# Optimization experiments

Hardware: AMD Instinct MI355X
Metric: run time of the kernel (lower is better)

Reference implementation:

```python
import jax, jax.numpy as jnp
import numpy as np

C = 512
NUM_HEADS = 8
HEAD_DIM = C // NUM_HEADS
GROUPS = 32
EPS = 1e-5


def setup_inputs() -> dict:
    key = jax.random.key(0)
    ks = jax.random.split(key, 7)
    N, H, W = 16, 32, 32
    x = jax.random.normal(ks[0], (N, C, H, W), dtype=jnp.float32)
    norm_w = jax.random.normal(ks[1], (C,), dtype=jnp.float32) * 0.02 + 1.0
    norm_b = jax.random.normal(ks[2], (C,), dtype=jnp.float32) * 0.02
    qkv_w = jax.random.normal(ks[3], (3 * C, C), dtype=jnp.float32) * (1.0 / np.sqrt(C))
    qkv_b = jax.random.normal(ks[4], (3 * C,), dtype=jnp.float32) * 0.02
    proj_w = jax.random.normal(ks[5], (C, C), dtype=jnp.float32) * (1.0 / np.sqrt(C))
    proj_b = jax.random.normal(ks[6], (C,), dtype=jnp.float32) * 0.02
    return {"x": x, "norm_w": norm_w, "norm_b": norm_b, "qkv_w": qkv_w,
            "qkv_b": qkv_b, "proj_w": proj_w, "proj_b": proj_b}


def _group_norm(x, w, b):
    N, Cc, H, W = x.shape
    xg = x.reshape(N, GROUPS, Cc // GROUPS, H, W)
    mean = xg.mean(axis=(2, 3, 4), keepdims=True)
    var = xg.var(axis=(2, 3, 4), keepdims=True)
    xg = (xg - mean) * jax.lax.rsqrt(var + EPS)
    return xg.reshape(N, Cc, H, W) * w[None, :, None, None] + b[None, :, None, None]


def reference(x, norm_w, norm_b, qkv_w, qkv_b, proj_w, proj_b):
    N, Cc, H, W = x.shape
    S = H * W
    h = _group_norm(x, norm_w, norm_b)
    # 1x1 conv == per-pixel linear over channels
    qkv = jnp.einsum('nchw,oc->nohw', h, qkv_w) + qkv_b[None, :, None, None]
    q, k, v = jnp.split(qkv, 3, axis=1)  # each [N, C, H, W]
    # [N, heads, head_dim, S]
    q = q.reshape(N, NUM_HEADS, HEAD_DIM, S)
    k = k.reshape(N, NUM_HEADS, HEAD_DIM, S)
    v = v.reshape(N, NUM_HEADS, HEAD_DIM, S)
    scale = HEAD_DIM ** -0.5
    attn = jnp.einsum('nhds,nhdt->nhst', q, k) * scale  # [N,heads,S,S]
    attn = jax.nn.softmax(attn, axis=-1)
    out = jnp.einsum('nhst,nhdt->nhds', attn, v)  # [N,heads,head_dim,S]
    out = out.reshape(N, Cc, H, W)
    out = jnp.einsum('nchw,oc->nohw', out, proj_w) + proj_b[None, :, None, None]
    return out + x
```

## Files before the change

### kernel.cpp

```cpp
#include <hip/hip_runtime.h>
#include <cstdint>
#include <cstddef>

typedef unsigned short u16;
typedef __attribute__((ext_vector_type(8))) short bf16x8;
typedef __attribute__((ext_vector_type(4))) short bf16x4;
typedef __attribute__((ext_vector_type(4))) float f32x4;
typedef __attribute__((ext_vector_type(16))) float f32x16;
typedef __attribute__((ext_vector_type(4))) unsigned short u16x4;

#define NB 16
#define CD 512
#define SD 1024
#define NH 8
#define HD 64

__device__ __forceinline__ u16 f2bf(float f) {
    unsigned u = __float_as_uint(f);
    u += 0x7FFF + ((u >> 16) & 1);
    return (u16)(u >> 16);
}
__device__ __forceinline__ unsigned cvt_pk(float lo, float hi) {
    unsigned r;
    asm("v_cvt_pk_bf16_f32 %0, %1, %2" : "=v"(r) : "v"(lo), "v"(hi));
    return r;
}
__device__ __forceinline__ void gload16(const void* g, void* l) {
    __builtin_amdgcn_global_load_lds(
        (const __attribute__((address_space(1))) void*)g,
        (__attribute__((address_space(3))) void*)l, 16, 0, 0);
}

__global__ __launch_bounds__(256) void cvt_kernel(
    const float* __restrict__ s, u16* __restrict__ d, int n)
{
    int i = (blockIdx.x * 256 + threadIdx.x) * 4;
    if (i >= n) return;
    float4 v = *reinterpret_cast<const float4*>(s + i);
    u16x4 o = { f2bf(v.x), f2bf(v.y), f2bf(v.z), f2bf(v.w) };
    *reinterpret_cast<u16x4*>(d + i) = o;
}

__global__ __launch_bounds__(256) void gn_kernel(
    const float* __restrict__ x, const float* __restrict__ w,
    const float* __restrict__ b, u16* __restrict__ h)
{
    const int n = blockIdx.x >> 5, g = blockIdx.x & 31;
    const size_t base = ((size_t)n * CD + g * 16) * SD;
    const float4* xp = reinterpret_cast<const float4*>(x + base);

    float4 vals[16];
    float sum = 0.f, ss = 0.f;
#pragma unroll
    for (int i = 0; i < 16; ++i) {
        float4 v = xp[threadIdx.x + (i << 8)];
        vals[i] = v;
        sum += v.x + v.y + v.z + v.w;
        ss  += v.x*v.x + v.y*v.y + v.z*v.z + v.w*v.w;
    }
#pragma unroll
    for (int off = 32; off > 0; off >>= 1) {
        sum += __shfl_down(sum, off);
        ss  += __shfl_down(ss,  off);
    }
    __shared__ float rs[4], rq[4];
    const int wid = threadIdx.x >> 6, lane = threadIdx.x & 63;
    if (lane == 0) { rs[wid] = sum; rq[wid] = ss; }
    __syncthreads();
    const float tsum = rs[0] + rs[1] + rs[2] + rs[3];
    const float tss  = rq[0] + rq[1] + rq[2] + rq[3];
    const float mean = tsum * (1.0f / 16384.0f);
    const float var  = tss * (1.0f / 16384.0f) - mean * mean;
    const float inv  = rsqrtf(var + 1e-5f);

    u16* hp = h + ((size_t)n * SD + 4 * threadIdx.x) * CD + g * 16;
#pragma unroll
    for (int i = 0; i < 16; ++i) {
        const float A  = inv * w[g * 16 + i];
        const float Bc = b[g * 16 + i] - mean * A;
        float4 v = vals[i];
        hp[i]          = f2bf(v.x * A + Bc);
        hp[CD + i]     = f2bf(v.y * A + Bc);
        hp[2 * CD + i] = f2bf(v.z * A + Bc);
        hp[3 * CD + i] = f2bf(v.w * A + Bc);
    }
}

__global__ __launch_bounds__(256) void mfma_gemm(
    const u16* __restrict__ Wb, const u16* __restrict__ act,
    const float* __restrict__ bias, const float* __restrict__ resid,
    void* __restrict__ outp, u16* __restrict__ vtout, int M, int mode)
{
    const int nb = blockIdx.z, m0 = blockIdx.y * 128, s0 = blockIdx.x * 128;
    __shared__ u16 Al[128 * 64];
    __shared__ u16 Bl[128 * 64];
    const int tid = threadIdx.x, wv = tid >> 6, ln = tid & 63;
    const int wm = wv >> 1, wn = wv & 1, lr = ln & 15, lg = ln >> 4;

    const f32x4 zero = {0.f, 0.f, 0.f, 0.f};
    f32x4 acc[4][4];
#pragma unroll
    for (int i = 0; i < 4; ++i)
#pragma unroll
        for (int j = 0; j < 4; ++j) acc[i][j] = zero;

    const u16* Ab = Wb + (size_t)m0 * CD;
    const u16* Bb = act + ((size_t)nb * SD + s0) * CD;

    for (int k0 = 0; k0 < CD; k0 += 64) {
        __syncthreads();
#pragma unroll
        for (int r = 0; r < 4; ++r) {
            const int gi = (r * 4 + wv) * 64 + ln;
            const int row = gi >> 3, gc = gi & 7;
            const int sg = ((gc ^ (row & 7)) * 8);
            gload16(Ab + (size_t)row * CD + k0 + sg, Al + gi * 8);
            gload16(Bb + (size_t)row * CD + k0 + sg, Bl + gi * 8);
        }
        __syncthreads();

        bf16x8 af[4][2], bfr[4][2];
#pragma unroll
        for (int mi = 0; mi < 4; ++mi) {
            const int row = wm * 64 + mi * 16 + lr;
#pragma unroll
            for (int kc = 0; kc < 2; ++kc)
                af[mi][kc] = *reinterpret_cast<const bf16x8*>(
                    Al + row * 64 + (((kc * 4 + lg) ^ (row & 7)) * 8));
        }
#pragma unroll
        for (int nj = 0; nj < 4; ++nj) {
            const int row = wn * 64 + nj * 16 + lr;
#pragma unroll
            for (int kc = 0; kc < 2; ++kc)
                bfr[nj][kc] = *reinterpret_cast<const bf16x8*>(
                    Bl + row * 64 + (((kc * 4 + lg) ^ (row & 7)) * 8));
        }
#pragma unroll
        for (int kc = 0; kc < 2; ++kc)
#pragma unroll
            for (int mi = 0; mi < 4; ++mi)
#pragma unroll
                for (int nj = 0; nj < 4; ++nj)
                    acc[mi][nj] = __builtin_amdgcn_mfma_f32_16x16x32_bf16(
                        af[mi][kc], bfr[nj][kc], acc[mi][nj], 0, 0, 0);
    }

    if (mode == 0) {
        if (m0 < 1024) {
            u16* o = (u16*)outp;
#pragma unroll
            for (int mi = 0; mi < 4; ++mi)
#pragma unroll
                for (int r = 0; r < 4; ++r) {
                    const int m = m0 + wm * 64 + mi * 16 + lg * 4 + r;
                    const float bi = bias[m];
#pragma unroll
                    for (int nj = 0; nj < 4; ++nj) {
                        const int s = s0 + wn * 64 + nj * 16 + lr;
                        o[((size_t)nb * SD + s) * 1024 + m] = f2bf(acc[mi][nj][r] + bi);
                    }
                }
        } else {
#pragma unroll
            for (int mi = 0; mi < 4; ++mi)
#pragma unroll
                for (int r = 0; r < 4; ++r) {
                    const int m = m0 + wm * 64 + mi * 16 + lg * 4 + r;
                    const float bi = bias[m];
#pragma unroll
                    for (int nj = 0; nj < 4; ++nj) {
                        const int s = s0 + wn * 64 + nj * 16 + lr;
                        vtout[((size_t)nb * 512 + (m - 1024)) * SD + s] = f2bf(acc[mi][nj][r] + bi);
                    }
                }
        }
    } else {
        float* o = (float*)outp;
#pragma unroll
        for (int mi = 0; mi < 4; ++mi)
#pragma unroll
            for (int r = 0; r < 4; ++r) {
                const int m = m0 + wm * 64 + mi * 16 + lg * 4 + r;
                const float bi = bias[m];
#pragma unroll
                for (int nj = 0; nj < 4; ++nj) {
                    const int s = s0 + wn * 64 + nj * 16 + lr;
                    const size_t idx = ((size_t)nb * M + m) * SD + s;
                    o[idx] = acc[mi][nj][r] + bi + resid[idx];
                }
            }
    }
}

__global__ __launch_bounds__(512) void attn_mfma(
    const u16* __restrict__ qk, const u16* __restrict__ vt, u16* __restrict__ ao)
{
    const int nh = blockIdx.y, n = nh >> 3, hh = nh & 7;
    const int q0 = blockIdx.x << 8;
    const int tid = threadIdx.x, wv = tid >> 6, ln = tid & 63;
    const int lq = ln & 31, hi = ln >> 5;

    __shared__ u16 Kl[2][64 * 64];
    __shared__ u16 Vl[2][64 * 64];

    const u16* Qb = qk + (size_t)n * SD * 1024 + hh * HD;
    const u16* Kb = Qb + 512;
    const u16* Vb = vt + ((size_t)n * 512 + hh * HD) * SD;

    bf16x8 qf[4];
    {
        const u16* qp = Qb + (size_t)(q0 + wv * 32 + lq) * 1024 + hi * 8;
#pragma unroll
        for (int ks = 0; ks < 4; ++ks)
            qf[ks] = *reinterpret_cast<const bf16x8*>(qp + ks * 16);
    }

    f32x16 of0 = {}, of1 = {};
    float mrun = -INFINITY, lrun = 0.f;

    const int srow = tid >> 3, sgc = tid & 7;
    const int ssw = (sgc ^ (srow & 7)) * 8;
    const u16* Ksrc = Kb + (size_t)srow * 1024 + ssw;
    const u16* Vsrc = Vb + (size_t)srow * SD + ssw;

    gload16(Ksrc, &Kl[0][tid * 8]);
    gload16(Vsrc, &Vl[0][tid * 8]);
    __syncthreads();

    int cur = 0;
    for (int tt = 0; tt < 16; ++tt) {
        if (tt < 15) {
            const int t1 = (tt + 1) << 6;
            gload16(Ksrc + (size_t)t1 * 1024, &Kl[cur ^ 1][tid * 8]);
            gload16(Vsrc + t1, &Vl[cur ^ 1][tid * 8]);
        }
        f32x16 st0 = {}, st1 = {};
        const u16* Kc = &Kl[cur][0];
#pragma unroll
        for (int ks = 0; ks < 4; ++ks) {
            const int g = (((ks * 2 + hi) ^ (lq & 7)) * 8);
            bf16x8 k0 = *reinterpret_cast<const bf16x8*>(Kc + lq * 64 + g);
            bf16x8 k1 = *reinterpret_cast<const bf16x8*>(Kc + (32 + lq) * 64 + g);
            st0 = __builtin_amdgcn_mfma_f32_32x32x16_bf16(k0, qf[ks], st0, 0, 0, 0);
            st1 = __builtin_amdgcn_mfma_f32_32x32x16_bf16(k1, qf[ks], st1, 0, 0, 0);
        }
        float mx = st0[0];
#pragma unroll
        for (int r = 1; r < 16; ++r) mx = fmaxf(mx, st0[r]);
#pragma unroll
        for (int r = 0; r < 16; ++r) mx = fmaxf(mx, st1[r]);
        mx = fmaxf(mx, __shfl_xor(mx, 32));
        const float mn = fmaxf(mrun, mx * 0.125f);
        const float al = __expf(mrun - mn);
        mrun = mn;
        float ps = 0.f;
        float p0[16], p1[16];
#pragma unroll
        for (int r = 0; r < 16; ++r) { p0[r] = __expf(st0[r] * 0.125f - mn); ps += p0[r]; }
#pragma unroll
        for (int r = 0; r < 16; ++r) { p1[r] = __expf(st1[r] * 0.125f - mn); ps += p1[r]; }
        ps += __shfl_xor(ps, 32);
        lrun = lrun * al + ps;
#pragma unroll
        for (int r = 0; r < 16; ++r) { of0[r] *= al; of1[r] *= al; }

        const u16* Vc = &Vl[cur][0];
#pragma unroll
        for (int ks = 0; ks < 4; ++ks) {
            union { unsigned w[4]; bf16x8 v; } pf;
            const int rb = (ks & 1) * 8;
            if (ks < 2) {
                pf.w[0] = cvt_pk(p0[rb + 0], p0[rb + 1]);
                pf.w[1] = cvt_pk(p0[rb + 2], p0[rb + 3]);
                pf.w[2] = cvt_pk(p0[rb + 4], p0[rb + 5]);
                pf.w[3] = cvt_pk(p0[rb + 6], p0[rb + 7]);
            } else {
                pf.w[0] = cvt_pk(p1[rb + 0], p1[rb + 1]);
                pf.w[1] = cvt_pk(p1[rb + 2], p1[rb + 3]);
                pf.w[2] = cvt_pk(p1[rb + 4], p1[rb + 5]);
                pf.w[3] = cvt_pk(p1[rb + 6], p1[rb + 7]);
            }
            const int e0 = ((2 * ks) ^ (lq & 7)) * 8 + hi * 4;
            const int e1 = ((2 * ks + 1) ^ (lq & 7)) * 8 + hi * 4;
            union { bf16x4 h[2]; bf16x8 v; } vf0, vf1;
            vf0.h[0] = *reinterpret_cast<const bf16x4*>(Vc + lq * 64 + e0);
            vf0.h[1] = *reinterpret_cast<const bf16x4*>(Vc + lq * 64 + e1);
            vf1.h[0] = *reinterpret_cast<const bf16x4*>(Vc + (32 + lq) * 64 + e0);
            vf1.h[1] = *reinterpret_cast<const bf16x4*>(Vc + (32 + lq) * 64 + e1);
            of0 = __builtin_amdgcn_mfma_f32_32x32x16_bf16(vf0.v, pf.v, of0, 0, 0, 0);
            of1 = __builtin_amdgcn_mfma_f32_32x32x16_bf16(vf1.v, pf.v, of1, 0, 0, 0);
        }
        __syncthreads();
        cur ^= 1;
    }

    const float inv = 1.0f / lrun;
    u16* op = ao + ((size_t)n * SD + q0 + wv * 32 + lq) * CD + hh * HD;
#pragma unroll
    for (int g = 0; g < 4; ++g) {
        u16x4 o0, o1;
#pragma unroll
        for (int e = 0; e < 4; ++e) {
            o0[e] = f2bf(of0[g * 4 + e] * inv);
            o1[e] = f2bf(of1[g * 4 + e] * inv);
        }
        const int d0 = g * 8 + hi * 4;
        *reinterpret_cast<u16x4*>(op + d0) = o0;
        *reinterpret_cast<u16x4*>(op + 32 + d0) = o1;
    }
}

extern "C" void kernel_launch(void* const* d_in, const int* in_sizes, int n_in,
                              void* d_out, int out_size, void* d_ws, size_t ws_size,
                              hipStream_t stream)
{
    const float* x      = (const float*)d_in[0];
    const float* norm_w = (const float*)d_in[1];
    const float* norm_b = (const float*)d_in[2];
    const float* qkv_w  = (const float*)d_in[3];
    const float* qkv_b  = (const float*)d_in[4];
    const float* proj_w = (const float*)d_in[5];
    const float* proj_b = (const float*)d_in[6];

    u16* h   = (u16*)d_ws;
    u16* qkb = h + (size_t)NB * SD * CD;
    u16* vtb = qkb + (size_t)NB * SD * 1024;
    u16* ao  = vtb + (size_t)NB * 512 * SD;
    u16* wq  = ao + (size_t)NB * SD * CD;
    u16* wp  = wq + (size_t)1536 * CD;

    hipLaunchKernelGGL(cvt_kernel, dim3(768), dim3(256), 0, stream, qkv_w, wq, 1536 * CD);
    hipLaunchKernelGGL(cvt_kernel, dim3(256), dim3(256), 0, stream, proj_w, wp, CD * CD);
    hipLaunchKernelGGL(gn_kernel, dim3(NB * 32), dim3(256), 0, stream, x, norm_w, norm_b, h);
    hipLaunchKernelGGL(mfma_gemm, dim3(8, 12, NB), dim3(256), 0, stream,
                       wq, h, qkv_b, (const float*)nullptr, (void*)qkb, vtb, 1536, 0);
    hipLaunchKernelGGL(attn_mfma, dim3(SD / 256, NB * NH), dim3(512), 0, stream,
                       qkb, vtb, ao);
    hipLaunchKernelGGL(mfma_gemm, dim3(8, 4, NB), dim3(256), 0, stream,
                       wp, ao, proj_b, x, (void*)d_out, (u16*)nullptr, 512, 1);
}
```

Before: 225.0 us.

## Fold softmax scale into Q, use exp2 with lazy rescale, vectorize GEMM epilogues

The QKV GEMM epilogue now multiplies Q by scale*log2(e) and writes four channels at once as packed vectors. The attention kernel then uses raw v_exp_f32 (exp2) without per-element scaling. It also skips the running-max rescale unless the new max exceeds the old one by more than 8, in which case the accumulators may grow up to 2^8 before the final normalisation. In the projection GEMM the MFMA operands are swapped so each lane holds contiguous spatial outputs, making the residual read and output store float4. s_setprio is raised around the MFMA blocks to favour matrix issue.

```diff
diff --git a/kernel.cpp b/kernel.cpp
--- a/kernel.cpp
+++ b/kernel.cpp
@@ -15,6 +15,8 @@
 #define NH 8
 #define HD 64
 
+#define QSCL 0.18033688011112042f
+
 __device__ __forceinline__ u16 f2bf(float f) {
     unsigned u = __float_as_uint(f);
     u += 0x7FFF + ((u >> 16) & 1);
@@ -23,6 +25,11 @@
 __device__ __forceinline__ unsigned cvt_pk(float lo, float hi) {
     unsigned r;
     asm("v_cvt_pk_bf16_f32 %0, %1, %2" : "=v"(r) : "v"(lo), "v"(hi));
+    return r;
+}
+__device__ __forceinline__ float exp2v(float x) {
+    float r;
+    asm("v_exp_f32 %0, %1" : "=v"(r) : "v"(x));
     return r;
 }
 __device__ __forceinline__ void gload16(const void* g, void* l) {
@@ -136,31 +143,40 @@
                 bfr[nj][kc] = *reinterpret_cast<const bf16x8*>(
                     Bl + row * 64 + (((kc * 4 + lg) ^ (row & 7)) * 8));
         }
+        __builtin_amdgcn_s_setprio(1);
 #pragma unroll
         for (int kc = 0; kc < 2; ++kc)
 #pragma unroll
             for (int mi = 0; mi < 4; ++mi)
 #pragma unroll
-                for (int nj = 0; nj < 4; ++nj)
-                    acc[mi][nj] = __builtin_amdgcn_mfma_f32_16x16x32_bf16(
-                        af[mi][kc], bfr[nj][kc], acc[mi][nj], 0, 0, 0);
+                for (int nj = 0; nj < 4; ++nj) {
+                    if (mode == 0)
+                        acc[mi][nj] = __builtin_amdgcn_mfma_f32_16x16x32_bf16(
+                            af[mi][kc], bfr[nj][kc], acc[mi][nj], 0, 0, 0);
+                    else
+                        acc[mi][nj] = __builtin_amdgcn_mfma_f32_16x16x32_bf16(
+                            bfr[mi][kc], af[nj][kc], acc[mi][nj], 0, 0, 0);
+                }
+        __builtin_amdgcn_s_setprio(0);
     }
 
     if (mode == 0) {
         if (m0 < 1024) {
             u16* o = (u16*)outp;
-#pragma unroll
-            for (int mi = 0; mi < 4; ++mi)
-#pragma unroll
-                for (int r = 0; r < 4; ++r) {
-                    const int m = m0 + wm * 64 + mi * 16 + lg * 4 + r;
-                    const float bi = bias[m];
-#pragma unroll
-                    for (int nj = 0; nj < 4; ++nj) {
-                        const int s = s0 + wn * 64 + nj * 16 + lr;
-                        o[((size_t)nb * SD + s) * 1024 + m] = f2bf(acc[mi][nj][r] + bi);
-                    }
+            const float sc = (m0 < 512) ? QSCL : 1.0f;
+#pragma unroll
+            for (int mi = 0; mi < 4; ++mi) {
+                const int mb = m0 + wm * 64 + mi * 16 + lg * 4;
+#pragma unroll
+                for (int nj = 0; nj < 4; ++nj) {
+                    const int s = s0 + wn * 64 + nj * 16 + lr;
+                    u16x4 pack;
+#pragma unroll
+                    for (int r = 0; r < 4; ++r)
+                        pack[r] = f2bf((acc[mi][nj][r] + bias[mb + r]) * sc);
+                    *reinterpret_cast<u16x4*>(o + ((size_t)nb * SD + s) * 1024 + mb) = pack;
                 }
+            }
         } else {
 #pragma unroll
             for (int mi = 0; mi < 4; ++mi)
@@ -178,17 +194,20 @@
     } else {
         float* o = (float*)outp;
 #pragma unroll
-        for (int mi = 0; mi < 4; ++mi)
-#pragma unroll
-            for (int r = 0; r < 4; ++r) {
-                const int m = m0 + wm * 64 + mi * 16 + lg * 4 + r;
+        for (int i = 0; i < 4; ++i)
+#pragma unroll
+            for (int j = 0; j < 4; ++j) {
+                const int m = m0 + wm * 64 + j * 16 + lr;
+                const int s = s0 + wn * 64 + i * 16 + lg * 4;
                 const float bi = bias[m];
-#pragma unroll
-                for (int nj = 0; nj < 4; ++nj) {
-                    const int s = s0 + wn * 64 + nj * 16 + lr;
-                    const size_t idx = ((size_t)nb * M + m) * SD + s;
-                    o[idx] = acc[mi][nj][r] + bi + resid[idx];
-                }
+                const size_t idx = ((size_t)nb * M + m) * SD + s;
+                float4 r4 = *reinterpret_cast<const float4*>(resid + idx);
+                float4 v;
+                v.x = acc[i][j][0] + bi + r4.x;
+                v.y = acc[i][j][1] + bi + r4.y;
+                v.z = acc[i][j][2] + bi + r4.z;
+                v.w = acc[i][j][3] + bi + r4.w;
+                *reinterpret_cast<float4*>(o + idx) = v;
             }
     }
 }
@@ -237,6 +256,7 @@
         }
         f32x16 st0 = {}, st1 = {};
         const u16* Kc = &Kl[cur][0];
+        __builtin_amdgcn_s_setprio(1);
 #pragma unroll
         for (int ks = 0; ks < 4; ++ks) {
             const int g = (((ks * 2 + hi) ^ (lq & 7)) * 8);
@@ -245,27 +265,32 @@
             st0 = __builtin_amdgcn_mfma_f32_32x32x16_bf16(k0, qf[ks], st0, 0, 0, 0);
             st1 = __builtin_amdgcn_mfma_f32_32x32x16_bf16(k1, qf[ks], st1, 0, 0, 0);
         }
+        __builtin_amdgcn_s_setprio(0);
         float mx = st0[0];
 #pragma unroll
         for (int r = 1; r < 16; ++r) mx = fmaxf(mx, st0[r]);
 #pragma unroll
         for (int r = 0; r < 16; ++r) mx = fmaxf(mx, st1[r]);
         mx = fmaxf(mx, __shfl_xor(mx, 32));
-        const float mn = fmaxf(mrun, mx * 0.125f);
-        const float al = __expf(mrun - mn);
-        mrun = mn;
+        if (!__all(mx - mrun <= 8.0f)) {
+            const float mn = fmaxf(mrun, mx);
+            const float al = exp2v(mrun - mn);
+            mrun = mn;
+            lrun *= al;
+#pragma unroll
+            for (int r = 0; r < 16; ++r) { of0[r] *= al; of1[r] *= al; }
+        }
         float ps = 0.f;
         float p0[16], p1[16];
 #pragma unroll
-        for (int r = 0; r < 16; ++r) { p0[r] = __expf(st0[r] * 0.125f - mn); ps += p0[r]; }
-#pragma unroll
-        for (int r = 0; r < 16; ++r) { p1[r] = __expf(st1[r] * 0.125f - mn); ps += p1[r]; }
+        for (int r = 0; r < 16; ++r) { p0[r] = exp2v(st0[r] - mrun); ps += p0[r]; }
+#pragma unroll
+        for (int r = 0; r < 16; ++r) { p1[r] = exp2v(st1[r] - mrun); ps += p1[r]; }
         ps += __shfl_xor(ps, 32);
-        lrun = lrun * al + ps;
-#pragma unroll
-        for (int r = 0; r < 16; ++r) { of0[r] *= al; of1[r] *= al; }
+        lrun += ps;
 
         const u16* Vc = &Vl[cur][0];
+        __builtin_amdgcn_s_setprio(1);
 #pragma unroll
         for (int ks = 0; ks < 4; ++ks) {
             union { unsigned w[4]; bf16x8 v; } pf;
@@ -291,6 +316,7 @@
             of0 = __builtin_amdgcn_mfma_f32_32x32x16_bf16(vf0.v, pf.v, of0, 0, 0, 0);
             of1 = __builtin_amdgcn_mfma_f32_32x32x16_bf16(vf1.v, pf.v, of1, 0, 0, 0);
         }
+        __builtin_amdgcn_s_setprio(0);
         __syncthreads();
         cur ^= 1;
     }
```

Measured after the change: 274.5 us. +22.0%, slower.
